# Optimization experiments

Hardware: AMD Instinct MI355X
Metric: run time of the kernel (lower is better)

The kernel has to match this reference:

```python
import jax, jax.numpy as jnp
import numpy as np

N = 32768      # total nodes
E = 262144     # total edges (avg degree 8)
S = 128        # graph segments
B = 16         # batch entries
C = S // B     # segments per batch entry
NF, NC = 90, 36
OP, OD = 120, 64
D0, DX, GIN, GH = 190, 380, 256, 512


def setup_inputs() -> dict:
    key = jax.random.key(0)
    ks = jax.random.split(key, 16)
    rn = lambda k, shape, s=0.02: jax.random.normal(k, shape, jnp.float32) * s
    return {
        "node_features": jax.random.normal(ks[0], (N, NF), jnp.float32),
        "node_config_features": jax.random.normal(ks[1], (N, NC), jnp.float32),
        "emb_table": rn(ks[2], (OP, OD), 1.0),
        "w1": rn(ks[3], (DX, D0)), "b1": jnp.zeros((DX,), jnp.float32),
        "g1": jnp.ones((DX,), jnp.float32), "be1": jnp.zeros((DX,), jnp.float32),
        "w2": rn(ks[4], (GIN, DX)), "b2": jnp.zeros((GIN,), jnp.float32),
        "g2": jnp.ones((GIN,), jnp.float32), "be2": jnp.zeros((GIN,), jnp.float32),
        "wl1": rn(ks[5], (GH, GIN)), "bl1": jnp.zeros((GH,), jnp.float32), "wr1": rn(ks[6], (GH, GIN)),
        "wl2": rn(ks[7], (GH, GH)), "bl2": jnp.zeros((GH,), jnp.float32), "wr2": rn(ks[8], (GH, GH)),
        "wl3": rn(ks[9], (GH, GH)), "bl3": jnp.zeros((GH,), jnp.float32), "wr3": rn(ks[10], (GH, GH)),
        "wc": rn(ks[11], (1, GH)), "bc": jnp.zeros((1,), jnp.float32),
        "node_ops": jax.random.randint(ks[12], (N,), 0, OP),
        "edges": jax.random.randint(ks[13], (2, E), 0, N),
        # cumulative end indices, equal-size segments; batches = segment -> batch entry
        "node_separation": (jnp.arange(S, dtype=jnp.int32) + 1) * (N // S),
        "batches": jnp.repeat(jnp.arange(B, dtype=jnp.int32), C),
    }


def _leaky(x):
    return jnp.where(x >= 0, x, 0.01 * x)


def _graphwise_ln(x, seg_id, counts, gamma, beta):
    # per-graph-segment mean/var over all nodes and features, per-feature affine
    D = x.shape[1]
    s = jax.ops.segment_sum(jnp.sum(x, -1), seg_id, num_segments=S)
    ss = jax.ops.segment_sum(jnp.sum(x * x, -1), seg_id, num_segments=S)
    cnt = counts.astype(x.dtype) * D
    mean = s / cnt
    var = ss / cnt - mean * mean
    inv = jax.lax.rsqrt(var + 1e-5)
    return (x - mean[seg_id, None]) * inv[seg_id, None] * gamma + beta


def _pairnorm(x):
    # PyG PairNorm, scale=1: center over nodes, divide by sqrt(mean row norm^2)
    xc = x - jnp.mean(x, axis=0, keepdims=True)
    denom = 1e-5 + jnp.sqrt(jnp.mean(jnp.sum(xc * xc, -1)))
    return xc / denom


def _sage(x, src, dst, inv_deg, wl, bl, wr):
    # SAGEConv(mean): lin_l(mean_neighbors) + lin_r(x)
    agg = jax.ops.segment_sum(x[src], dst, num_segments=N) * inv_deg[:, None]
    return agg @ wl.T + bl + x @ wr.T


def reference(node_features, node_config_features, emb_table, w1, b1, g1, be1,
              w2, b2, g2, be2, wl1, bl1, wr1, wl2, bl2, wr2, wl3, bl3, wr3,
              wc, bc, node_ops, edges, node_separation, batches):
    seg_id = jnp.searchsorted(node_separation, jnp.arange(N), side="right")
    counts = jnp.diff(node_separation, prepend=0)
    src, dst = edges[0], edges[1]
    deg = jax.ops.segment_sum(jnp.ones((E,), jnp.float32), dst, num_segments=N)
    inv_deg = 1.0 / jnp.maximum(deg, 1.0)

    x = jnp.concatenate([node_features, node_config_features, emb_table[node_ops]], axis=1)
    # node_features_mlp: Linear -> LeakyReLU -> GLN -> Linear -> LeakyReLU -> GLN
    x = _graphwise_ln(_leaky(x @ w1.T + b1), seg_id, counts, g1, be1)
    x = _graphwise_ln(_leaky(x @ w2.T + b2), seg_id, counts, g2, be2)
    # GraphSAGE: 3 layers, PairNorm + ReLU after all but the last
    x = jax.nn.relu(_pairnorm(_sage(x, src, dst, inv_deg, wl1, bl1, wr1)))
    x = jax.nn.relu(_pairnorm(_sage(x, src, dst, inv_deg, wl2, bl2, wr2)))
    x = _sage(x, src, dst, inv_deg, wl3, bl3, wr3)
    # ragged per-segment sum pooling (replaces the python loop) -> [S, GH]
    seg_sums = jax.ops.segment_sum(x, seg_id, num_segments=S)
    # batches = repeat(arange(B), C) and segments are in order -> reshape groups
    agg = seg_sums.reshape(B, C, GH)
    out = agg @ wc.T + bc  # [B, C, 1]
    return jnp.squeeze(out, 2)
```

## Files before the change

### kernel.cpp

```cpp
#include <hip/hip_runtime.h>
#include <hip/hip_bf16.h>

#define NN   32768
#define EE   262144
#define SS   128
#define NF_  90
#define NC_  36
#define OD_  64
#define D0_  190
#define DX_  380
#define GIN_ 256
#define GH_  512

typedef __attribute__((ext_vector_type(8))) short  s8v;
typedef __attribute__((ext_vector_type(4))) float  f4v;

typedef const __attribute__((address_space(1))) void* gas_ptr;
typedef __attribute__((address_space(3))) void*       las_ptr;

__device__ __forceinline__ float bf2f(unsigned u) {
  return __uint_as_float(u << 16);
}
__device__ __forceinline__ unsigned short f2bf(float f) {
  unsigned u = __float_as_uint(f);
  u += 0x7FFFu + ((u >> 16) & 1u);
  return (unsigned short)(u >> 16);
}
__device__ __forceinline__ unsigned pack2(float a, float b) {
  return ((unsigned)f2bf(b) << 16) | (unsigned)f2bf(a);
}

__global__ void deg_count(const int* __restrict__ dst, int* __restrict__ deg) {
  int e = blockIdx.x * 256 + threadIdx.x;
  if (e < EE) atomicAdd(&deg[dst[e]], 1);
}

__global__ __launch_bounds__(256) void blk_sum_k(const int* __restrict__ deg,
                                                 int* __restrict__ bsum) {
  __shared__ int buf[256];
  int tid = threadIdx.x;
  buf[tid] = deg[blockIdx.x * 256 + tid];
  __syncthreads();
  for (int off = 128; off > 0; off >>= 1) {
    if (tid < off) buf[tid] += buf[tid + off];
    __syncthreads();
  }
  if (tid == 0) bsum[blockIdx.x] = buf[0];
}

__global__ __launch_bounds__(128) void blk_scan_k(const int* __restrict__ bsum,
                                                  int* __restrict__ boff) {
  __shared__ int buf[128];
  int tid = threadIdx.x;
  int v = bsum[tid];
  buf[tid] = v;
  __syncthreads();
  for (int d = 1; d < 128; d <<= 1) {
    int t = (tid >= d) ? buf[tid - d] : 0;
    __syncthreads();
    if (tid >= d) buf[tid] += t;
    __syncthreads();
  }
  boff[tid] = buf[tid] - v;
}

__global__ __launch_bounds__(256) void offsets_k(const int* __restrict__ deg,
                                                 const int* __restrict__ boff,
                                                 int* __restrict__ offsets,
                                                 float* __restrict__ inv_deg) {
  __shared__ int buf[256];
  int tid = threadIdx.x;
  int i = blockIdx.x * 256 + tid;
  int v = deg[i];
  buf[tid] = v;
  __syncthreads();
  for (int d = 1; d < 256; d <<= 1) {
    int t = (tid >= d) ? buf[tid - d] : 0;
    __syncthreads();
    if (tid >= d) buf[tid] += t;
    __syncthreads();
  }
  offsets[i] = boff[blockIdx.x] + buf[tid] - v;
  inv_deg[i] = 1.0f / fmaxf((float)v, 1.0f);
  if (i == 0) offsets[NN] = EE;
}

__global__ void bucket_k(const int* __restrict__ src, const int* __restrict__ dst,
                         const int* __restrict__ offsets, int* __restrict__ cursor,
                         int* __restrict__ srcs) {
  int e = blockIdx.x * 256 + threadIdx.x;
  if (e < EE) {
    int d = dst[e];
    int pos = offsets[d] + atomicAdd(&cursor[d], 1);
    srcs[pos] = src[e];
  }
}

#define P1 73728
#define P2 172032
#define P3 434176
#define P4 958464
#define P5 1482752

__global__ __launch_bounds__(256) void prep_all(
    const float* __restrict__ nf, const float* __restrict__ ncf,
    const float* __restrict__ emb, const int* __restrict__ ops,
    const float* __restrict__ w1, const float* __restrict__ w2,
    const float* __restrict__ wl1, const float* __restrict__ wr1,
    const float* __restrict__ wl2, const float* __restrict__ wr2,
    const float* __restrict__ wl3, const float* __restrict__ wr3,
    unsigned short* __restrict__ w1b, unsigned short* __restrict__ w2b,
    unsigned short* __restrict__ wc1, unsigned short* __restrict__ wc2,
    unsigned short* __restrict__ wc3,
    unsigned short* __restrict__ x0,
    float* __restrict__ stat_all, float* __restrict__ outp,
    const float* __restrict__ bc)
{
  const int T = 4096 * 256;
  int gidx = blockIdx.x * 256 + threadIdx.x;
  for (int i = gidx; i < 2560; i += T) stat_all[i] = 0.0f;
  if (gidx < SS) outp[gidx] = bc[0];
  for (int i = gidx; i < P5; i += T) {
    if (i < P1) {
      int r = i / 192, c = i - r * 192;
      w1b[i] = f2bf((r < DX_ && c < D0_) ? w1[r * D0_ + c] : 0.0f);
    } else if (i < P2) {
      int j = i - P1;
      int r = j / 384, c = j - r * 384;
      w2b[j] = f2bf((c < DX_) ? w2[r * DX_ + c] : 0.0f);
    } else if (i < P3) {
      int j = i - P2;
      int r = j >> 9, c = j & 511;
      wc1[j] = f2bf((c < 256) ? wl1[r * 256 + c] : wr1[r * 256 + (c - 256)]);
    } else if (i < P4) {
      int j = i - P3;
      int r = j >> 10, c = j & 1023;
      wc2[j] = f2bf((c < 512) ? wl2[r * 512 + c] : wr2[r * 512 + (c - 512)]);
    } else {
      int j = i - P4;
      int r = j >> 10, c = j & 1023;
      wc3[j] = f2bf((c < 512) ? wl3[r * 512 + c] : wr3[r * 512 + (c - 512)]);
    }
  }
  for (int i = gidx; i < NN * 192; i += T) {
    int n = i / 192;
    int c = i - n * 192;
    float v;
    if (c < NF_)            v = nf[n * NF_ + c];
    else if (c < NF_ + NC_) v = ncf[n * NC_ + (c - NF_)];
    else if (c < D0_)       v = emb[ops[n] * OD_ + (c - (NF_ + NC_))];
    else                    v = 0.0f;
    x0[i] = f2bf(v);
  }
}

__device__ __forceinline__ void stage64(const unsigned short* __restrict__ G, int ld,
                                        int base_row, int k0,
                                        unsigned short* __restrict__ lds, int tid) {
#pragma unroll
  for (int i = 0; i < 4; ++i) {
    int c = tid + i * 256;
    int row = c & 127;
    int koff = c >> 7;
    const unsigned short* src = G + (size_t)(base_row + row) * ld + k0 + koff * 8;
    unsigned short* dst = lds + koff * 1024 + row * 8;
    __builtin_amdgcn_global_load_lds((gas_ptr)(const void*)src, (las_ptr)(void*)dst,
                                     16, 0, 0);
  }
}

__global__ __launch_bounds__(256) void mfma_gemm(
    const unsigned short* __restrict__ A, int lda,
    const unsigned short* __restrict__ B, int ldb, int K,
    const float* __restrict__ bias,
    float* __restrict__ C, int ldc, int Nreal, int mode, int swz,
    float* __restrict__ st0, float* __restrict__ st1,
    const float* __restrict__ wcp, float* __restrict__ outp)
{
  __shared__ unsigned short As[8192];
  __shared__ unsigned short Bs[8192];
  int tid = threadIdx.x;
  int lane = tid & 63;
  int w = tid >> 6;
  int wm = (w & 1) * 64;
  int wn = (w >> 1) * 64;
  int bm, bn;
  if (swz) {
    int L = blockIdx.x;
    int xcd = L & 7;
    int s = L >> 3;
    bn = (s & 3) * 128;
    bm = ((s >> 2) * 8 + xcd) * 128;
  } else {
    bm = blockIdx.y * 128;
    bn = blockIdx.x * 128;
  }
  int quad = lane >> 4;
  int r16 = lane & 15;

  f4v acc[4][4] = {};

  for (int k0 = 0; k0 < K; k0 += 64) {
    stage64(A, lda, bm, k0, As, tid);
    stage64(B, ldb, bn, k0, Bs, tid);
    __syncthreads();
#pragma unroll
    for (int s = 0; s < 2; ++s) {
      s8v af[4], bfr[4];
#pragma unroll
      for (int mi = 0; mi < 4; ++mi)
        af[mi] = *(const s8v*)&As[(s * 4 + quad) * 1024 + (wm + mi * 16 + r16) * 8];
#pragma unroll
      for (int ni = 0; ni < 4; ++ni)
        bfr[ni] = *(const s8v*)&Bs[(s * 4 + quad) * 1024 + (wn + ni * 16 + r16) * 8];
#pragma unroll
      for (int mi = 0; mi < 4; ++mi)
#pragma unroll
        for (int ni = 0; ni < 4; ++ni)
          acc[mi][ni] = __builtin_amdgcn_mfma_f32_16x16x32_bf16(
              af[mi], bfr[ni], acc[mi][ni], 0, 0, 0);
    }
    __syncthreads();
  }

  float* red = (float*)As;
  float* cs  = (float*)Bs;
  float* css = ((float*)Bs) + 128;

  int seg = bm >> 8;

  if (mode == 1) {
    float lsum = 0.0f, lssq = 0.0f;
#pragma unroll
    for (int mi = 0; mi < 4; ++mi) {
      int gm = bm + wm + mi * 16 + quad * 4;
#pragma unroll
      for (int ni = 0; ni < 4; ++ni) {
        int gn = bn + wn + ni * 16 + r16;
        if (gn < Nreal) {
          float bv = bias[gn];
#pragma unroll
          for (int r = 0; r < 4; ++r) {
            float v = acc[mi][ni][r] + bv;
            v = (v >= 0.0f) ? v : 0.01f * v;
            C[(size_t)(gm + r) * ldc + gn] = v;
            lsum += v;
            lssq += v * v;
          }
        }
      }
    }
    red[tid] = lsum;
    __syncthreads();
    for (int off = 128; off > 0; off >>= 1) {
      if (tid < off) red[tid] += red[tid + off];
      __syncthreads();
    }
    if (tid == 0) atomicAdd(&st0[seg], red[0]);
    __syncthreads();
    red[tid] = lssq;
    __syncthreads();
    for (int off = 128; off > 0; off >>= 1) {
      if (tid < off) red[tid] += red[tid + off];
      __syncthreads();
    }
    if (tid == 0) atomicAdd(&st1[seg], red[0]);
  } else if (mode == 2) {
    if (tid < 128) { cs[tid] = 0.0f; css[tid] = 0.0f; }
    __syncthreads();
#pragma unroll
    for (int ni = 0; ni < 4; ++ni) {
      int col = wn + ni * 16 + r16;
      int gn = bn + col;
      float bv = bias[gn];
      float psum = 0.0f, pssq = 0.0f;
#pragma unroll
      for (int mi = 0; mi < 4; ++mi) {
        int gm = bm + wm + mi * 16 + quad * 4;
#pragma unroll
        for (int r = 0; r < 4; ++r) {
          float v = acc[mi][ni][r] + bv;
          C[(size_t)(gm + r) * ldc + gn] = v;
          psum += v;
          pssq += v * v;
        }
      }
      atomicAdd(&cs[col], psum);
      atomicAdd(&css[col], pssq);
    }
    __syncthreads();
    if (tid < 128) {
      atomicAdd(&st0[bn + tid], cs[tid]);
      atomicAdd(&st1[bn + tid], css[tid]);
    }
  } else {
    float part = 0.0f;
#pragma unroll
    for (int ni = 0; ni < 4; ++ni) {
      int gn = bn + wn + ni * 16 + r16;
      float bv = bias[gn];
      float wv = wcp[gn];
      float colsum = 0.0f;
#pragma unroll
      for (int mi = 0; mi < 4; ++mi)
#pragma unroll
        for (int r = 0; r < 4; ++r)
          colsum += acc[mi][ni][r] + bv;
      part += colsum * wv;
    }
    red[tid] = part;
    __syncthreads();
    for (int off = 128; off > 0; off >>= 1) {
      if (tid < off) red[tid] += red[tid + off];
      __syncthreads();
    }
    if (tid == 0) atomicAdd(&outp[seg], red[0]);
  }
}

__global__ __launch_bounds__(256) void gln_apply_v(
    const float* __restrict__ x, int D, int Dp, int lanes4, int rpb,
    const float* __restrict__ seg_sum, const float* __restrict__ seg_ssq,
    const float* __restrict__ g, const float* __restrict__ be,
    unsigned short* __restrict__ out, int ldo, int co) {
  int tid = threadIdx.x;
  int ri = tid / lanes4;
  if (ri >= rpb) return;
  int f4 = tid - ri * lanes4;
  int r = blockIdx.x * rpb + ri;
  int s = r >> 8;
  float cnt = 256.0f * (float)D;
  float m = seg_sum[s] / cnt;
  float var = seg_ssq[s] / cnt - m * m;
  float inv = rsqrtf(var + 1e-5f);
  int c0 = f4 * 4;
  float4 v = ((const float4*)(x + (size_t)r * Dp))[f4];
  float o0 = (c0 + 0 < D) ? ((v.x - m) * inv * g[c0 + 0] + be[c0 + 0]) : 0.0f;
  float o1 = (c0 + 1 < D) ? ((v.y - m) * inv * g[c0 + 1] + be[c0 + 1]) : 0.0f;
  float o2 = (c0 + 2 < D) ? ((v.z - m) * inv * g[c0 + 2] + be[c0 + 2]) : 0.0f;
  float o3 = (c0 + 3 < D) ? ((v.w - m) * inv * g[c0 + 3] + be[c0 + 3]) : 0.0f;
  uint2 o;
  o.x = pack2(o0, o1);
  o.y = pack2(o2, o3);
  ((uint2*)(out + (size_t)r * ldo + co))[f4] = o;
}

__device__ __forceinline__ void acc8(uint4 v, float& a0, float& a1, float& a2,
                                     float& a3, float& a4, float& a5,
                                     float& a6, float& a7) {
  a0 += bf2f(v.x & 0xffffu); a1 += bf2f(v.x >> 16);
  a2 += bf2f(v.y & 0xffffu); a3 += bf2f(v.y >> 16);
  a4 += bf2f(v.z & 0xffffu); a5 += bf2f(v.z >> 16);
  a6 += bf2f(v.w & 0xffffu); a7 += bf2f(v.w >> 16);
}

__global__ __launch_bounds__(256) void aggregate8(
    const unsigned short* __restrict__ xs, int ldu4, int cb4, int cba4, int L8,
    unsigned short* __restrict__ aggs,
    const int* __restrict__ offsets, const int* __restrict__ srcs,
    const float* __restrict__ inv_deg) {
  int tid = threadIdx.x;
  int b = blockIdx.x;
  int xcd = b & 7;
  int x = b >> 3;
  int lb = L8 - 1;
  int mtile = ((x >> lb) << 3) + xcd;
  int within = x & ((1 << lb) - 1);
  int n = mtile * 128 + (within << (8 - L8)) + (tid >> L8);
  int f8 = tid & ((1 << L8) - 1);
  int start = offsets[n], end = offsets[n + 1];
  float wgt = inv_deg[n];
  const uint4* xb = (const uint4*)xs;
  float a0 = 0, a1 = 0, a2 = 0, a3 = 0, a4 = 0, a5 = 0, a6 = 0, a7 = 0;
  int e = start;
  for (; e + 4 <= end; e += 4) {
    uint4 v0 = xb[(size_t)srcs[e] * ldu4 + cb4 + f8];
    uint4 v1 = xb[(size_t)srcs[e + 1] * ldu4 + cb4 + f8];
    uint4 v2 = xb[(size_t)srcs[e + 2] * ldu4 + cb4 + f8];
    uint4 v3 = xb[(size_t)srcs[e + 3] * ldu4 + cb4 + f8];
    acc8(v0, a0, a1, a2, a3, a4, a5, a6, a7);
    acc8(v1, a0, a1, a2, a3, a4, a5, a6, a7);
    acc8(v2, a0, a1, a2, a3, a4, a5, a6, a7);
    acc8(v3, a0, a1, a2, a3, a4, a5, a6, a7);
  }
  for (; e < end; ++e) {
    uint4 v = xb[(size_t)srcs[e] * ldu4 + cb4 + f8];
    acc8(v, a0, a1, a2, a3, a4, a5, a6, a7);
  }
  uint4 o;
  o.x = pack2(a0 * wgt, a1 * wgt);
  o.y = pack2(a2 * wgt, a3 * wgt);
  o.z = pack2(a4 * wgt, a5 * wgt);
  o.w = pack2(a6 * wgt, a7 * wgt);
  ((uint4*)aggs)[(size_t)n * ldu4 + cba4 + f8] = o;
}

__global__ __launch_bounds__(512) void pn_finalize(const float* __restrict__ colsum,
                                                   const float* __restrict__ colssq,
                                                   float* __restrict__ mu,
                                                   float* __restrict__ invd) {
  int f = threadIdx.x;
  float m = colsum[f] / (float)NN;
  mu[f] = m;
  float t = colssq[f] / (float)NN - m * m;
  __shared__ float buf[512];
  buf[f] = t;
  __syncthreads();
  for (int off = 256; off > 0; off >>= 1) {
    if (f < off) buf[f] += buf[f + off];
    __syncthreads();
  }
  if (f == 0) invd[0] = 1.0f / (1e-5f + sqrtf(fmaxf(buf[0], 0.0f)));
}

__global__ __launch_bounds__(256) void pn_apply_v(const float* __restrict__ y,
                                                  const float* __restrict__ mu,
                                                  const float* __restrict__ invd,
                                                  unsigned short* __restrict__ xb,
                                                  int ldou2, int cou2) {
  int t = threadIdx.x;
  int b = blockIdx.x;
  int xcd = b & 7;
  int x = b >> 3;
  int mtile = ((x >> 6) << 3) + xcd;
  int within = x & 63;
  int r = mtile * 128 + within * 2 + (t >> 7);
  int f4 = t & 127;
  float id = invd[0];
  float4 v = ((const float4*)(y + (size_t)r * GH_))[f4];
  float4 m = ((const float4*)mu)[f4];
  float v0 = fmaxf((v.x - m.x) * id, 0.0f);
  float v1 = fmaxf((v.y - m.y) * id, 0.0f);
  float v2 = fmaxf((v.z - m.z) * id, 0.0f);
  float v3 = fmaxf((v.w - m.w) * id, 0.0f);
  uint2 o;
  o.x = pack2(v0, v1);
  o.y = pack2(v2, v3);
  ((uint2*)xb)[(size_t)r * ldou2 + cou2 + f4] = o;
}

extern "C" void kernel_launch(void* const* d_in, const int* in_sizes, int n_in,
                              void* d_out, int out_size, void* d_ws, size_t ws_size,
                              hipStream_t stream) {
  const float* node_features = (const float*)d_in[0];
  const float* node_config   = (const float*)d_in[1];
  const float* emb_table     = (const float*)d_in[2];
  const float* w1  = (const float*)d_in[3];
  const float* b1  = (const float*)d_in[4];
  const float* g1  = (const float*)d_in[5];
  const float* be1 = (const float*)d_in[6];
  const float* w2  = (const float*)d_in[7];
  const float* b2  = (const float*)d_in[8];
  const float* g2  = (const float*)d_in[9];
  const float* be2 = (const float*)d_in[10];
  const float* wl1 = (const float*)d_in[11];
  const float* bl1 = (const float*)d_in[12];
  const float* wr1 = (const float*)d_in[13];
  const float* wl2 = (const float*)d_in[14];
  const float* bl2 = (const float*)d_in[15];
  const float* wr2 = (const float*)d_in[16];
  const float* wl3 = (const float*)d_in[17];
  const float* bl3 = (const float*)d_in[18];
  const float* wr3 = (const float*)d_in[19];
  const float* wc  = (const float*)d_in[20];
  const float* bc  = (const float*)d_in[21];
  const int* node_ops = (const int*)d_in[22];
  const int* edges    = (const int*)d_in[23];
  float* out = (float*)d_out;

  char* ws = (char*)d_ws;
  size_t off = 0;
  auto alloc = [&](size_t bytes) -> void* {
    void* p = ws + off;
    off += (bytes + 255) & ~(size_t)255;
    return p;
  };

  int*   deg_i   = (int*)alloc(NN * 4);
  int*   cursor  = (int*)alloc(NN * 4);
  int*   offsets = (int*)alloc((NN + 1) * 4);
  int*   srcs    = (int*)alloc(EE * 4);
  int*   bsum    = (int*)alloc(SS * 4);
  int*   boff    = (int*)alloc(SS * 4);
  float* inv_deg = (float*)alloc(NN * 4);
  float* stat_all= (float*)alloc(2560 * 4);
  float* mu      = (float*)alloc(512 * 4);
  float* invd    = (float*)alloc(256);
  unsigned short* w1b = (unsigned short*)alloc((size_t)384 * 192 * 2);
  unsigned short* w2b = (unsigned short*)alloc((size_t)256 * 384 * 2);
  unsigned short* wc1 = (unsigned short*)alloc((size_t)512 * 512 * 2);
  unsigned short* wc2 = (unsigned short*)alloc((size_t)512 * 1024 * 2);
  unsigned short* wc3 = (unsigned short*)alloc((size_t)512 * 1024 * 2);
  unsigned short* X0  = (unsigned short*)alloc((size_t)NN * 192 * 2);
  unsigned short* H1  = (unsigned short*)alloc((size_t)NN * 384 * 2);
  unsigned short* XC1 = (unsigned short*)alloc((size_t)NN * 512 * 2);
  unsigned short* XC2 = (unsigned short*)alloc((size_t)NN * 1024 * 2);
  float*          Y   = (float*)alloc((size_t)NN * 512 * 4);

  const int* esrc = edges;
  const int* edst = edges + EE;

  float* gln1s = stat_all;        float* gln1q = stat_all + 128;
  float* gln2s = stat_all + 256;  float* gln2q = stat_all + 384;
  float* pn1s  = stat_all + 512;  float* pn1q  = stat_all + 1024;
  float* pn2s  = stat_all + 1536; float* pn2q  = stat_all + 2048;

  hipMemsetAsync(deg_i, 0, (size_t)NN * 4 * 2, stream);

  deg_count<<<EE / 256, 256, 0, stream>>>(edst, deg_i);
  blk_sum_k<<<NN / 256, 256, 0, stream>>>(deg_i, bsum);
  blk_scan_k<<<1, 128, 0, stream>>>(bsum, boff);
  offsets_k<<<NN / 256, 256, 0, stream>>>(deg_i, boff, offsets, inv_deg);
  bucket_k<<<EE / 256, 256, 0, stream>>>(esrc, edst, offsets, cursor, srcs);

  prep_all<<<4096, 256, 0, stream>>>(node_features, node_config, emb_table, node_ops,
                                     w1, w2, wl1, wr1, wl2, wr2, wl3, wr3,
                                     w1b, w2b, wc1, wc2, wc3,
                                     X0, stat_all, out, bc);

  {
    dim3 g(3, 256);
    mfma_gemm<<<g, 256, 0, stream>>>(X0, 192, w1b, 192, 192,
                                     b1, Y, 384, DX_, 1, 0,
                                     gln1s, gln1q, nullptr, nullptr);
  }
  gln_apply_v<<<NN / 2, 256, 0, stream>>>(Y, DX_, 384, 96, 2, gln1s, gln1q,
                                          g1, be1, H1, 384, 0);

  {
    dim3 g(2, 256);
    mfma_gemm<<<g, 256, 0, stream>>>(H1, 384, w2b, 384, 384,
                                     b2, Y, 256, GIN_, 1, 0,
                                     gln2s, gln2q, nullptr, nullptr);
  }
  gln_apply_v<<<NN / 4, 256, 0, stream>>>(Y, GIN_, 256, 64, 4, gln2s, gln2q,
                                          g2, be2, XC1, 512, 256);

  aggregate8<<<NN / 8, 256, 0, stream>>>(XC1, 64, 32, 0, 5, XC1,
                                         offsets, srcs, inv_deg);
  mfma_gemm<<<1024, 256, 0, stream>>>(XC1, 512, wc1, 512, 512,
                                      bl1, Y, 512, GH_, 2, 1,
                                      pn1s, pn1q, nullptr, nullptr);
  pn_finalize<<<1, 512, 0, stream>>>(pn1s, pn1q, mu, invd);
  pn_apply_v<<<NN / 2, 256, 0, stream>>>(Y, mu, invd, XC2, 256, 128);

  aggregate8<<<NN / 4, 256, 0, stream>>>(XC2, 128, 64, 0, 6, XC2,
                                         offsets, srcs, inv_deg);
  mfma_gemm<<<1024, 256, 0, stream>>>(XC2, 1024, wc2, 1024, 1024,
                                      bl2, Y, 512, GH_, 2, 1,
                                      pn2s, pn2q, nullptr, nullptr);
  pn_finalize<<<1, 512, 0, stream>>>(pn2s, pn2q, mu, invd);
  pn_apply_v<<<NN / 2, 256, 0, stream>>>(Y, mu, invd, XC2, 256, 128);

  aggregate8<<<NN / 4, 256, 0, stream>>>(XC2, 128, 64, 0, 6, XC2,
                                         offsets, srcs, inv_deg);
  mfma_gemm<<<1024, 256, 0, stream>>>(XC2, 1024, wc3, 1024, 1024,
                                      bl3, nullptr, 512, GH_, 3, 1,
                                      nullptr, nullptr, wc, out);
}
```

Measured before the change: 600.7 us.

## Store GEMM intermediate outputs in bf16 and simplify aggregation block mapping

```diff
diff --git a/kernel.cpp b/kernel.cpp
--- a/kernel.cpp
+++ b/kernel.cpp
@@ -173,7 +173,7 @@
     const unsigned short* __restrict__ A, int lda,
     const unsigned short* __restrict__ B, int ldb, int K,
     const float* __restrict__ bias,
-    float* __restrict__ C, int ldc, int Nreal, int mode, int swz,
+    unsigned short* __restrict__ C, int ldc, int Nreal, int mode, int swz,
     float* __restrict__ st0, float* __restrict__ st1,
     const float* __restrict__ wcp, float* __restrict__ outp)
 {
@@ -243,7 +243,7 @@
           for (int r = 0; r < 4; ++r) {
             float v = acc[mi][ni][r] + bv;
             v = (v >= 0.0f) ? v : 0.01f * v;
-            C[(size_t)(gm + r) * ldc + gn] = v;
+            C[(size_t)(gm + r) * ldc + gn] = f2bf(v);
             lsum += v;
             lssq += v * v;
           }
@@ -280,7 +280,7 @@
 #pragma unroll
         for (int r = 0; r < 4; ++r) {
           float v = acc[mi][ni][r] + bv;
-          C[(size_t)(gm + r) * ldc + gn] = v;
+          C[(size_t)(gm + r) * ldc + gn] = f2bf(v);
           psum += v;
           pssq += v * v;
         }
@@ -319,7 +319,7 @@
 }
 
 __global__ __launch_bounds__(256) void gln_apply_v(
-    const float* __restrict__ x, int D, int Dp, int lanes4, int rpb,
+    const unsigned short* __restrict__ y, int D, int Dp, int lanes4, int rpb,
     const float* __restrict__ seg_sum, const float* __restrict__ seg_ssq,
     const float* __restrict__ g, const float* __restrict__ be,
     unsigned short* __restrict__ out, int ldo, int co) {
@@ -334,11 +334,13 @@
   float var = seg_ssq[s] / cnt - m * m;
   float inv = rsqrtf(var + 1e-5f);
   int c0 = f4 * 4;
-  float4 v = ((const float4*)(x + (size_t)r * Dp))[f4];
-  float o0 = (c0 + 0 < D) ? ((v.x - m) * inv * g[c0 + 0] + be[c0 + 0]) : 0.0f;
-  float o1 = (c0 + 1 < D) ? ((v.y - m) * inv * g[c0 + 1] + be[c0 + 1]) : 0.0f;
-  float o2 = (c0 + 2 < D) ? ((v.z - m) * inv * g[c0 + 2] + be[c0 + 2]) : 0.0f;
-  float o3 = (c0 + 3 < D) ? ((v.w - m) * inv * g[c0 + 3] + be[c0 + 3]) : 0.0f;
+  uint2 v = ((const uint2*)(y + (size_t)r * Dp))[f4];
+  float y0 = bf2f(v.x & 0xffffu), y1 = bf2f(v.x >> 16);
+  float y2 = bf2f(v.y & 0xffffu), y3 = bf2f(v.y >> 16);
+  float o0 = (c0 + 0 < D) ? ((y0 - m) * inv * g[c0 + 0] + be[c0 + 0]) : 0.0f;
+  float o1 = (c0 + 1 < D) ? ((y1 - m) * inv * g[c0 + 1] + be[c0 + 1]) : 0.0f;
+  float o2 = (c0 + 2 < D) ? ((y2 - m) * inv * g[c0 + 2] + be[c0 + 2]) : 0.0f;
+  float o3 = (c0 + 3 < D) ? ((y3 - m) * inv * g[c0 + 3] + be[c0 + 3]) : 0.0f;
   uint2 o;
   o.x = pack2(o0, o1);
   o.y = pack2(o2, o3);
@@ -360,30 +362,20 @@
     const int* __restrict__ offsets, const int* __restrict__ srcs,
     const float* __restrict__ inv_deg) {
   int tid = threadIdx.x;
-  int b = blockIdx.x;
-  int xcd = b & 7;
-  int x = b >> 3;
-  int lb = L8 - 1;
-  int mtile = ((x >> lb) << 3) + xcd;
-  int within = x & ((1 << lb) - 1);
-  int n = mtile * 128 + (within << (8 - L8)) + (tid >> L8);
+  int n = (blockIdx.x << (8 - L8)) + (tid >> L8);
   int f8 = tid & ((1 << L8) - 1);
   int start = offsets[n], end = offsets[n + 1];
   float wgt = inv_deg[n];
   const uint4* xb = (const uint4*)xs;
   float a0 = 0, a1 = 0, a2 = 0, a3 = 0, a4 = 0, a5 = 0, a6 = 0, a7 = 0;
   int e = start;
-  for (; e + 4 <= end; e += 4) {
+  for (; e + 2 <= end; e += 2) {
     uint4 v0 = xb[(size_t)srcs[e] * ldu4 + cb4 + f8];
     uint4 v1 = xb[(size_t)srcs[e + 1] * ldu4 + cb4 + f8];
-    uint4 v2 = xb[(size_t)srcs[e + 2] * ldu4 + cb4 + f8];
-    uint4 v3 = xb[(size_t)srcs[e + 3] * ldu4 + cb4 + f8];
     acc8(v0, a0, a1, a2, a3, a4, a5, a6, a7);
     acc8(v1, a0, a1, a2, a3, a4, a5, a6, a7);
-    acc8(v2, a0, a1, a2, a3, a4, a5, a6, a7);
-    acc8(v3, a0, a1, a2, a3, a4, a5, a6, a7);
-  }
-  for (; e < end; ++e) {
+  }
+  if (e < end) {
     uint4 v = xb[(size_t)srcs[e] * ldu4 + cb4 + f8];
     acc8(v, a0, a1, a2, a3, a4, a5, a6, a7);
   }
@@ -413,26 +405,21 @@
   if (f == 0) invd[0] = 1.0f / (1e-5f + sqrtf(fmaxf(buf[0], 0.0f)));
 }
 
-__global__ __launch_bounds__(256) void pn_apply_v(const float* __restrict__ y,
+__global__ __launch_bounds__(256) void pn_apply_v(const unsigned short* __restrict__ y,
                                                   const float* __restrict__ mu,
                                                   const float* __restrict__ invd,
                                                   unsigned short* __restrict__ xb,
                                                   int ldou2, int cou2) {
   int t = threadIdx.x;
-  int b = blockIdx.x;
-  int xcd = b & 7;
-  int x = b >> 3;
-  int mtile = ((x >> 6) << 3) + xcd;
-  int within = x & 63;
-  int r = mtile * 128 + within * 2 + (t >> 7);
+  int r = blockIdx.x * 2 + (t >> 7);
   int f4 = t & 127;
   float id = invd[0];
-  float4 v = ((const float4*)(y + (size_t)r * GH_))[f4];
+  uint2 v = ((const uint2*)(y + (size_t)r * GH_))[f4];
   float4 m = ((const float4*)mu)[f4];
-  float v0 = fmaxf((v.x - m.x) * id, 0.0f);
-  float v1 = fmaxf((v.y - m.y) * id, 0.0f);
-  float v2 = fmaxf((v.z - m.z) * id, 0.0f);
-  float v3 = fmaxf((v.w - m.w) * id, 0.0f);
+  float v0 = fmaxf((bf2f(v.x & 0xffffu) - m.x) * id, 0.0f);
+  float v1 = fmaxf((bf2f(v.x >> 16)     - m.y) * id, 0.0f);
+  float v2 = fmaxf((bf2f(v.y & 0xffffu) - m.z) * id, 0.0f);
+  float v3 = fmaxf((bf2f(v.y >> 16)     - m.w) * id, 0.0f);
   uint2 o;
   o.x = pack2(v0, v1);
   o.y = pack2(v2, v3);
@@ -495,7 +482,7 @@
   unsigned short* H1  = (unsigned short*)alloc((size_t)NN * 384 * 2);
   unsigned short* XC1 = (unsigned short*)alloc((size_t)NN * 512 * 2);
   unsigned short* XC2 = (unsigned short*)alloc((size_t)NN * 1024 * 2);
-  float*          Y   = (float*)alloc((size_t)NN * 512 * 4);
+  unsigned short* Y   = (unsigned short*)alloc((size_t)NN * 512 * 2);
 
   const int* esrc = edges;
   const int* edst = edges + EE;
```

Result: no change. 601.4 us (+0.1%).
